# Optimization experiments

Measured on AMD Instinct MI355X. Metric: run time of the kernel, lower is better.

## Reference

```python
import jax, jax.numpy as jnp
import numpy as np
import math

B, T, E = 1, 2048, 1024
H = 8                      # num_heads
D = E // H // 2            # head_dim = 64
LAMBDA_INIT = 0.8 - 0.6 * math.exp(-0.3 * 1)  # depth=1
SCALE_BASE = 512.0
THETA = 10000.0


def _rope_tables(T, d):
    # lucidrains rotary-embedding-torch, use_xpos=True, interleaved pairs
    inv_freq = 1.0 / (THETA ** (jnp.arange(0, d, 2, dtype=jnp.float32) / d))
    pos = jnp.arange(T, dtype=jnp.float32)
    freqs = pos[:, None] * inv_freq[None, :]            # (T, d/2)
    freqs = jnp.repeat(freqs, 2, axis=-1)               # (T, d) interleaved
    sv = (jnp.arange(0, d, 2, dtype=jnp.float32) + 0.4 * d) / (1.4 * d)
    power = (pos - T // 2) / SCALE_BASE
    scale = sv[None, :] ** power[:, None]               # (T, d/2)
    scale = jnp.concatenate([scale, scale], axis=-1)    # (T, d)
    return freqs, scale


def _rotate_half(x):
    # interleaved rotate: (..., d) pairs (x1, x2) -> (-x2, x1)
    x1 = x[..., 0::2]
    x2 = x[..., 1::2]
    return jnp.stack([-x2, x1], axis=-1).reshape(x.shape)


def _apply_rope(t, freqs, scale):
    # t: (B, T, h, d); freqs/scale: (T, d) broadcast over heads
    f = freqs[None, :, None, :]
    s = scale[None, :, None, :]
    return t * jnp.cos(f) * s + _rotate_half(t) * jnp.sin(f) * s


def setup_inputs() -> dict:
    key = jax.random.key(0)
    ks = jax.random.split(key, 9)
    w = 0.02
    return {
        "x": jax.random.normal(ks[0], (B, T, E), dtype=jnp.float32),
        "Wq": jax.random.normal(ks[1], (E, E), dtype=jnp.float32) * w,
        "Wk": jax.random.normal(ks[2], (E, E), dtype=jnp.float32) * w,
        "Wv": jax.random.normal(ks[3], (E, E), dtype=jnp.float32) * w,
        "Wo": jax.random.normal(ks[4], (E, E), dtype=jnp.float32) * w,
        "lambda_q1": jax.random.normal(ks[5], (D,), dtype=jnp.float32) * 0.1,
        "lambda_k1": jax.random.normal(ks[6], (D,), dtype=jnp.float32) * 0.1,
        "lambda_q2": jax.random.normal(ks[7], (D,), dtype=jnp.float32) * 0.1,
        "lambda_k2": jax.random.normal(ks[8], (D,), dtype=jnp.float32) * 0.1,
    }


def reference(x, Wq, Wk, Wv, Wo, lambda_q1, lambda_k1, lambda_q2, lambda_k2):
    b, t, e = x.shape
    scaling = D ** -0.5

    q = (x @ Wq.T).reshape(b, t, 2 * H, D)
    k = (x @ Wk.T).reshape(b, t, 2 * H, D)   # n_rep = 1
    v = (x @ Wv.T).reshape(b, t, H, 2 * D)

    freqs, scale = _rope_tables(t, D)
    q = _apply_rope(q, freqs, scale)
    k = _apply_rope(k, freqs, 1.0 / scale)   # xpos: keys use scale**-1

    q = jnp.transpose(q, (0, 2, 1, 3)) * scaling   # (B, 2H, T, D)
    k = jnp.transpose(k, (0, 2, 1, 3))             # (B, 2H, T, D)
    v = jnp.transpose(v, (0, 2, 1, 3))             # (B, H, T, 2D)

    scores = jnp.einsum('bhtd,bhsd->bhts', q, k)
    probs = jax.nn.softmax(scores.astype(jnp.float32), axis=-1).astype(scores.dtype)

    lam1 = jnp.exp(jnp.sum(lambda_q1 * lambda_k1))
    lam2 = jnp.exp(jnp.sum(lambda_q2 * lambda_k2))
    lam = lam1 - lam2 + LAMBDA_INIT

    probs = probs.reshape(b, H, 2, t, t)
    diff = probs[:, :, 0] - lam * probs[:, :, 1]   # (B, H, T, T)

    attn = jnp.einsum('bhts,bhsd->bhtd', diff, v)  # (B, H, T, 2D)
    # RMSNorm (no affine), eps=1e-5
    attn = attn * jax.lax.rsqrt(jnp.mean(attn * attn, axis=-1, keepdims=True) + 1e-5)
    attn = attn * (1.0 - LAMBDA_INIT)

    attn = jnp.transpose(attn, (0, 2, 1, 3)).reshape(b, t, e)
    return attn @ Wo.T
```

## Files before the change

kernel.cpp:

```cpp
#include <hip/hip_runtime.h>
#include <hip/hip_bf16.h>

typedef __hip_bfloat16 bf16;
typedef _Float16 f16;
typedef __attribute__((ext_vector_type(8))) __bf16 bf16x8;
typedef __attribute__((ext_vector_type(8))) _Float16 f16x8;
typedef __attribute__((ext_vector_type(4))) _Float16 f16x4;
typedef __attribute__((ext_vector_type(4))) float floatx4;
typedef __attribute__((ext_vector_type(16))) float floatx16;

#define T_SEQ 2048
#define EMB   1024
#define LAMBDA_INIT 0.35550906759096926f

__device__ __forceinline__ bf16 f2bf(float f) {
  unsigned u;
  __builtin_memcpy(&u, &f, 4);
  u += 0x7FFF + ((u >> 16) & 1);
  unsigned short h = (unsigned short)(u >> 16);
  bf16 r;
  __builtin_memcpy(&r, &h, 2);
  return r;
}

__device__ __forceinline__ int cvtpk_bf16(float lo, float hi) {
  int r;
  asm("v_cvt_pk_bf16_f32 %0, %1, %2" : "=v"(r) : "v"(lo), "v"(hi));
  return r;
}

__device__ __forceinline__ void permswap(int& a, int& b) {
  asm volatile("v_permlane32_swap_b32 %0, %1" : "+v"(a), "+v"(b));
}

__device__ __forceinline__ void gl_lds16(const void* g, void* l) {
  __builtin_amdgcn_global_load_lds((const __attribute__((address_space(1))) void*)g,
                                   (__attribute__((address_space(3))) void*)l, 16, 0, 0);
}

__device__ __forceinline__ floatx4 mfma_h(f16x8 a, f16x8 b, floatx4 c) {
  return __builtin_amdgcn_mfma_f32_16x16x32_f16(a, b, c, 0, 0, 0);
}
__device__ __forceinline__ floatx16 mfma32_h(f16x8 a, f16x8 b, floatx16 c) {
  return __builtin_amdgcn_mfma_f32_32x32x16_f16(a, b, c, 0, 0, 0);
}
__device__ __forceinline__ floatx16 mfma32_bf(bf16x8 a, bf16x8 b, floatx16 c) {
  return __builtin_amdgcn_mfma_f32_32x32x16_bf16(a, b, c, 0, 0, 0);
}

__global__ __launch_bounds__(256) void convert_kernel(
    const float* __restrict__ x,  const float* __restrict__ wq,
    const float* __restrict__ wk, const float* __restrict__ wv,
    const float* __restrict__ wo,
    f16* __restrict__ xf, f16* __restrict__ wqf, f16* __restrict__ wkf,
    f16* __restrict__ wvf, f16* __restrict__ wof)
{
  int b = blockIdx.x;
  const float* src; f16* dst; long off;
  if      (b < 2048) { src = x;  dst = xf;  off = (long)b * 1024; }
  else if (b < 3072) { src = wq; dst = wqf; off = (long)(b - 2048) * 1024; }
  else if (b < 4096) { src = wk; dst = wkf; off = (long)(b - 3072) * 1024; }
  else if (b < 5120) { src = wv; dst = wvf; off = (long)(b - 4096) * 1024; }
  else               { src = wo; dst = wof; off = (long)(b - 5120) * 1024; }
  long i = off + threadIdx.x * 4;
  float4 v = *(const float4*)(src + i);
  f16x4 o;
  o.x = (f16)v.x; o.y = (f16)v.y; o.z = (f16)v.z; o.w = (f16)v.w;
  *(f16x4*)(dst + i) = o;
}

template <int MODE>
__device__ __forceinline__ void gemm64x128_f16(
    const f16* __restrict__ A_, const f16* __restrict__ B_,
    void* C0v, int K, int ldc, int m0, int n0, char* smem)
{
  f16* As = (f16*)smem;
  f16* Bs = (f16*)(smem + 8192);
  const int tid  = threadIdx.x;
  const int wave = tid >> 6, lane = tid & 63, quad = lane >> 4, l16 = lane & 15;
  const int mo = (wave & 1) << 5;
  const int no = (wave >> 1) << 6;

  floatx4 acc[2][4];
  #pragma unroll
  for (int i = 0; i < 2; i++)
    #pragma unroll
    for (int j = 0; j < 4; j++) { acc[i][j][0]=0.f; acc[i][j][1]=0.f; acc[i][j][2]=0.f; acc[i][j][3]=0.f; }

  const int srow = tid >> 3;
  const int ch   = (tid & 7) ^ (srow & 7);
  const long aoff = (long)(m0 + srow) * K + ch * 8;
  const long boff = (long)(n0 + srow) * K + ch * 8;
  const int wb = wave << 10;

  for (int k0 = 0; k0 < K; k0 += 64) {
    #pragma unroll
    for (int rr = 0; rr < 2; rr++)
      gl_lds16(A_ + aoff + k0 + (long)rr * 32 * K, smem + wb + rr * 4096);
    #pragma unroll
    for (int rr = 0; rr < 4; rr++)
      gl_lds16(B_ + boff + k0 + (long)rr * 32 * K, smem + 8192 + wb + rr * 4096);
    __syncthreads();
    #pragma unroll
    for (int kt = 0; kt < 2; kt++) {
      f16x8 a[2], b[4];
      #pragma unroll
      for (int i = 0; i < 2; i++) {
        int m = mo + i * 16 + l16;
        a[i] = *(const f16x8*)(As + m * 64 + ((((kt << 2) | quad) ^ (m & 7)) << 3));
      }
      #pragma unroll
      for (int j = 0; j < 4; j++) {
        int n = no + j * 16 + l16;
        b[j] = *(const f16x8*)(Bs + n * 64 + ((((kt << 2) | quad) ^ (n & 7)) << 3));
      }
      #pragma unroll
      for (int i = 0; i < 2; i++)
        #pragma unroll
        for (int j = 0; j < 4; j++)
          acc[i][j] = mfma_h(a[i], b[j], acc[i][j]);
    }
    __syncthreads();
  }

  if (MODE == 1) {
    #pragma unroll
    for (int i = 0; i < 2; i++)
      #pragma unroll
      for (int j = 0; j < 4; j++)
        #pragma unroll
        for (int r = 0; r < 4; r++) {
          int row = m0 + mo + i * 16 + quad * 4 + r;
          int col = n0 + no + j * 16 + l16;
          ((float*)C0v)[(long)row * ldc + col] = acc[i][j][r];
        }
  } else {
    unsigned short* E = (unsigned short*)smem;
    #pragma unroll
    for (int i = 0; i < 2; i++)
      #pragma unroll
      for (int j = 0; j < 4; j++)
        #pragma unroll
        for (int r = 0; r < 4; r++) {
          int row = mo + i * 16 + quad * 4 + r;
          int col = no + j * 16 + l16;
          float v = acc[i][j][r];
          unsigned short bits;
          if (MODE == 0) {
            bf16 t = f2bf(v);
            __builtin_memcpy(&bits, &t, 2);
          } else {
            float p = __shfl_xor(v, 1, 64);
            int d = col & 63;
            float fr = (float)(m0 + row) * __expf((float)(d >> 1) * -0.28782313662425574f);
            float sn, cs;
            sincosf(fr, &sn, &cs);
            float rot = (col & 1) ? fmaf(v, cs, p * sn) : fmaf(v, cs, -p * sn);
            float power = (float)(m0 + row - 1024) * (1.0f / 512.0f);
            if (MODE == 3) power = -power;
            float sv = fmaf(2.0f, (float)(d & 31), 25.6f) * (1.0f / 89.6f);
            float s = __expf(power * __logf(sv));
            float ov = rot * s;
            if (MODE == 2) ov *= 0.125f;
            f16 t = (f16)ov;
            __builtin_memcpy(&bits, &t, 2);
          }
          E[row * 128 + col] = bits;
        }
    __syncthreads();
    const int rr0 = tid >> 4;
    const int c8  = (tid & 15) * 8;
    #pragma unroll
    for (int p2 = 0; p2 < 4; p2++) {
      int row = p2 * 16 + rr0;
      *(uint4*)((unsigned short*)C0v + (long)(m0 + row) * ldc + n0 + c8) =
          *(const uint4*)(E + row * 128 + c8);
    }
  }
}

__global__ __launch_bounds__(256) void qkv_gemm(
    const f16* __restrict__ xf,
    const f16* __restrict__ wqf, const f16* __restrict__ wkf,
    const f16* __restrict__ wvf,
    f16* __restrict__ qf, f16* __restrict__ kf, bf16* __restrict__ vt)
{
  __shared__ char smem[24576];
  int bid = blockIdx.x;
  if (bid < 256) {
    gemm64x128_f16<2>(xf, wqf, qf, 1024, 1024, (bid >> 3) * 64, (bid & 7) * 128, smem);
  } else if (bid < 512) {
    bid -= 256;
    gemm64x128_f16<3>(xf, wkf, kf, 1024, 1024, (bid >> 3) * 64, (bid & 7) * 128, smem);
  } else {
    bid -= 512;
    gemm64x128_f16<0>(wvf, xf, vt, 1024, 2048, (bid >> 4) * 64, (bid & 15) * 128, smem);
  }
}

__global__ __launch_bounds__(256) void out_gemm(const f16* __restrict__ attn,
                                                const f16* __restrict__ Wo,
                                                float* __restrict__ out)
{
  __shared__ char smem[24576];
  gemm64x128_f16<1>(attn, Wo, out, 1024, 1024,
                    (blockIdx.x >> 3) * 64, (blockIdx.x & 7) * 128, smem);
}

__global__ __launch_bounds__(256) void diff_attn(
    const f16* __restrict__ qf_, const f16* __restrict__ kf_,
    const bf16* __restrict__ vt,
    const float* __restrict__ lq1, const float* __restrict__ lk1,
    const float* __restrict__ lq2, const float* __restrict__ lk2,
    f16* __restrict__ attn)
{
  __shared__ char smem[65536];
  const int tid  = threadIdx.x;
  const int wave = tid >> 6, lane = tid & 63;
  const int l32 = lane & 31, lh = lane >> 5;
  const int h  = blockIdx.x & 7;
  const int qb = blockIdx.x >> 3;
  const int hl = wave >> 1;
  const int ws = wave & 1;
  const int hh = h * 2 + hl;
  const int t0 = qb * 32;

  float a1 = lq1[lane] * lk1[lane];
  float a2 = lq2[lane] * lk2[lane];
  #pragma unroll
  for (int off = 1; off < 64; off <<= 1) {
    a1 += __shfl_xor(a1, off, 64);
    a2 += __shfl_xor(a2, off, 64);
  }
  const float lam = __expf(a1) - __expf(a2) + LAMBDA_INIT;

  f16x8 qfr[4];
  {
    const f16* qrow = qf_ + (long)(t0 + l32) * EMB + hh * 64 + lh * 8;
    #pragma unroll
    for (int kt = 0; kt < 4; kt++) qfr[kt] = *(const f16x8*)(qrow + kt * 16);
  }

  floatx16 o[4];
  #pragma unroll
  for (int nt = 0; nt < 4; nt++)
    #pragma unroll
    for (int r = 0; r < 16; r++) o[nt][r] = 0.f;
  float lr0 = 0.f, lr1 = 0.f, lr2 = 0.f, lr3 = 0.f;

  const int srow = lane >> 3;
  const int ch   = (lane & 7) ^ srow;
  const f16*  kgp = kf_ + (long)(h * 2 + ws) * 64 + (long)srow * EMB + ch * 8;
  const bf16* vgp = vt + (long)(h * 128 + (wave - 2) * 64 + srow) * T_SEQ + ch * 8;
  const int kofs = wave * 8192;
  const int vofs = 16384 + (wave - 2) * 8192;

  if (wave < 2) {
    #pragma unroll
    for (int j = 0; j < 8; j++)
      gl_lds16(kgp + (long)j * 8 * EMB, smem + kofs + j * 1024);
  } else {
    #pragma unroll
    for (int j = 0; j < 8; j++)
      gl_lds16(vgp + (long)j * 8 * T_SEQ, smem + vofs + j * 1024);
  }

  for (int kb = 0; kb < T_SEQ; kb += 64) {
    const int cur = (kb >> 6) & 1;
    const char* sb = smem + cur * 32768;

    asm volatile("s_waitcnt vmcnt(0)" ::: "memory");
    asm volatile("s_barrier" ::: "memory");

    const f16*  Ks  = (const f16*)(sb + hl * 8192);
    const bf16* Vsb = (const bf16*)(sb + 16384);

    f16x8 kfr[4];
    #pragma unroll
    for (int kt = 0; kt < 4; kt++) {
      int krow = ws * 32 + l32;
      int c = kt * 2 + lh;
      kfr[kt] = *(const f16x8*)(Ks + krow * 64 + ((c ^ (krow & 7)) << 3));
    }
    bf16x8 vfr[4][2];
    #pragma unroll
    for (int nt = 0; nt < 4; nt++) {
      #pragma unroll
      for (int kt = 0; kt < 2; kt++) {
        int vrow = nt * 32 + l32;
        int c = ws * 4 + kt * 2 + lh;
        vfr[nt][kt] = *(const bf16x8*)(Vsb + vrow * 64 + ((c ^ (vrow & 7)) << 3));
      }
    }

    if (kb + 64 < T_SEQ) {
      char* nb = smem + (cur ^ 1) * 32768;
      if (wave < 2) {
        #pragma unroll
        for (int j = 0; j < 8; j++)
          gl_lds16(kgp + (long)(kb + 64) * EMB + (long)j * 8 * EMB,
                   nb + kofs + j * 1024);
      } else {
        #pragma unroll
        for (int j = 0; j < 8; j++)
          gl_lds16(vgp + (kb + 64) + (long)j * 8 * T_SEQ,
                   nb + vofs + j * 1024);
      }
    }

    floatx16 s;
    #pragma unroll
    for (int r = 0; r < 16; r++) s[r] = 0.f;
    #pragma unroll
    for (int kt = 0; kt < 4; kt++)
      s = mfma32_h(kfr[kt], qfr[kt], s);
    #pragma unroll
    for (int r = 0; r < 4; r++) {
      float p0 = __builtin_amdgcn_exp2f(
          fmaf(s[r], 1.4426950408889634f, -17.312340490667562f));
      float p1 = __builtin_amdgcn_exp2f(
          fmaf(s[r + 4], 1.4426950408889634f, -17.312340490667562f));
      float p2 = __builtin_amdgcn_exp2f(
          fmaf(s[r + 8], 1.4426950408889634f, -17.312340490667562f));
      float p3 = __builtin_amdgcn_exp2f(
          fmaf(s[r + 12], 1.4426950408889634f, -17.312340490667562f));
      s[r] = p0; s[r + 4] = p1; s[r + 8] = p2; s[r + 12] = p3;
      lr0 += p0; lr1 += p1; lr2 += p2; lr3 += p3;
    }
    bf16x8 pf[2];
    #pragma unroll
    for (int kt = 0; kt < 2; kt++) {
      const int b0 = kt * 8;
      int w0 = cvtpk_bf16(s[b0 + 0], s[b0 + 1]);
      int w1 = cvtpk_bf16(s[b0 + 2], s[b0 + 3]);
      int w2 = cvtpk_bf16(s[b0 + 4], s[b0 + 5]);
      int w3 = cvtpk_bf16(s[b0 + 6], s[b0 + 7]);
      permswap(w0, w2);
      permswap(w1, w3);
      union { int i[4]; bf16x8 v; } u;
      u.i[0] = w0; u.i[1] = w1; u.i[2] = w2; u.i[3] = w3;
      pf[kt] = u.v;
    }
    #pragma unroll
    for (int nt = 0; nt < 4; nt++) {
      #pragma unroll
      for (int kt = 0; kt < 2; kt++)
        o[nt] = mfma32_bf(pf[kt], vfr[nt][kt], o[nt]);
    }
  }
  __syncthreads();

  float lr = (lr0 + lr1) + (lr2 + lr3);
  float lrw = lr + __shfl_xor(lr, 32, 64);

  float* Cb = (float*)smem;
  float* Lb = (float*)(smem + 32768);

  if (ws == 1) {
    #pragma unroll
    for (int r = 0; r < 16; r++) {
      int m = (r & 3) + 8 * (r >> 2) + 4 * lh;
      #pragma unroll
      for (int nt = 0; nt < 4; nt++)
        Cb[hl * 4096 + m * 128 + nt * 32 + l32] = o[nt][r];
    }
  }
  if (lh == 0) Lb[ws * 64 + hl * 32 + l32] = lrw;
  __syncthreads();
  if (ws == 0) {
    #pragma unroll
    for (int r = 0; r < 16; r++) {
      int m = (r & 3) + 8 * (r >> 2) + 4 * lh;
      float inv = 1.0f / (Lb[hl * 32 + m] + Lb[64 + hl * 32 + m]);
      #pragma unroll
      for (int nt = 0; nt < 4; nt++)
        o[nt][r] = (o[nt][r] + Cb[hl * 4096 + m * 128 + nt * 32 + l32]) * inv;
    }
  }
  __syncthreads();
  if (hl == 1 && ws == 0) {
    #pragma unroll
    for (int r = 0; r < 16; r++) {
      int m = (r & 3) + 8 * (r >> 2) + 4 * lh;
      #pragma unroll
      for (int nt = 0; nt < 4; nt++)
        Cb[4096 + m * 128 + nt * 32 + l32] = o[nt][r];
    }
  }
  __syncthreads();
  if (hl == 0 && ws == 0) {
    float ss[16];
    #pragma unroll
    for (int r = 0; r < 16; r++) {
      int m = (r & 3) + 8 * (r >> 2) + 4 * lh;
      ss[r] = 0.f;
      #pragma unroll
      for (int nt = 0; nt < 4; nt++) {
        float v = o[nt][r] - lam * Cb[4096 + m * 128 + nt * 32 + l32];
        o[nt][r] = v;
        ss[r] += v * v;
      }
    }
    #pragma unroll
    for (int r = 0; r < 16; r++) {
      ss[r] += __shfl_xor(ss[r], 1, 64);
      ss[r] += __shfl_xor(ss[r], 2, 64);
      ss[r] += __shfl_xor(ss[r], 4, 64);
      ss[r] += __shfl_xor(ss[r], 8, 64);
      ss[r] += __shfl_xor(ss[r], 16, 64);
      float rms = rsqrtf(ss[r] * (1.0f / 128.0f) + 1e-5f) * (1.0f - LAMBDA_INIT);
      int m = (r & 3) + 8 * (r >> 2) + 4 * lh;
      #pragma unroll
      for (int nt = 0; nt < 4; nt++)
        attn[(long)(t0 + m) * EMB + h * 128 + nt * 32 + l32] = (f16)(o[nt][r] * rms);
    }
  }
}

extern "C" void kernel_launch(void* const* d_in, const int* in_sizes, int n_in,
                              void* d_out, int out_size, void* d_ws, size_t ws_size,
                              hipStream_t stream)
{
  (void)in_sizes; (void)n_in; (void)out_size; (void)ws_size;
  const float* x   = (const float*)d_in[0];
  const float* Wq  = (const float*)d_in[1];
  const float* Wk  = (const float*)d_in[2];
  const float* Wv  = (const float*)d_in[3];
  const float* Wo  = (const float*)d_in[4];
  const float* lq1 = (const float*)d_in[5];
  const float* lk1 = (const float*)d_in[6];
  const float* lq2 = (const float*)d_in[7];
  const float* lk2 = (const float*)d_in[8];
  float* out = (float*)d_out;

  const size_t TM = (size_t)T_SEQ * EMB;
  const size_t WM = (size_t)EMB * EMB;
  bf16* vtws = (bf16*)d_ws;
  f16*  aws  = (f16*)(vtws + TM);
  f16*  xf   = aws  + TM;
  f16*  wqf  = xf   + TM;
  f16*  wkf  = wqf  + WM;
  f16*  wvf  = wkf  + WM;
  f16*  wof  = wvf  + WM;
  f16*  qf   = wof  + WM;
  f16*  kf   = qf   + TM;

  convert_kernel<<<6144, 256, 0, stream>>>(x, Wq, Wk, Wv, Wo,
                                           xf, wqf, wkf, wvf, wof);
  qkv_gemm<<<768, 256, 0, stream>>>(xf, wqf, wkf, wvf, qf, kf, vtws);
  diff_attn<<<512, 256, 0, stream>>>(qf, kf, vtws, lq1, lk1, lq2, lk2, aws);
  out_gemm<<<256, 256, 0, stream>>>(aws, wof, out);
}
```

Before: 172.7 us.

## Use 128x128 double-buffered direct-to-LDS tiles for QKV projection GEMM

Adds a new 128x128 GEMM tile routine for the QKV projection. It uses BK=64, a swizzled LDS layout, global-to-LDS async loads and double buffering across k-steps, with the RoPE/xpos epilogue kept. The goal is to raise data reuse per block and overlap loads with MFMA work, halving the grid to 384 blocks. In exchange it uses 64KB of LDS and more accumulators per block, which may lower occupancy and gives fewer blocks to spread over the CUs.

```diff
diff --git a/kernel.cpp b/kernel.cpp
--- a/kernel.cpp
+++ b/kernel.cpp
@@ -134,67 +134,140 @@
           int col = n0 + no + j * 16 + l16;
           ((float*)C0v)[(long)row * ldc + col] = acc[i][j][r];
         }
-  } else {
-    unsigned short* E = (unsigned short*)smem;
-    #pragma unroll
-    for (int i = 0; i < 2; i++)
-      #pragma unroll
-      for (int j = 0; j < 4; j++)
+  }
+}
+
+template <int MODE>
+__device__ __forceinline__ void gemm128x128_f16(
+    const f16* __restrict__ A_, const f16* __restrict__ B_,
+    void* C0v, int K, int ldc, int m0, int n0, char* smem)
+{
+  const int tid  = threadIdx.x;
+  const int wave = tid >> 6, lane = tid & 63, quad = lane >> 4, l16 = lane & 15;
+  const int mo = wave << 5;
+
+  floatx4 acc[2][8];
+  #pragma unroll
+  for (int i = 0; i < 2; i++)
+    #pragma unroll
+    for (int j = 0; j < 8; j++) { acc[i][j][0]=0.f; acc[i][j][1]=0.f; acc[i][j][2]=0.f; acc[i][j][3]=0.f; }
+
+  const int srow = tid >> 3;
+  const int ch   = (tid & 7) ^ (srow & 7);
+  const long aoff = (long)(m0 + srow) * K + ch * 8;
+  const long boff = (long)(n0 + srow) * K + ch * 8;
+  const int wb = wave << 10;
+
+  #pragma unroll
+  for (int j = 0; j < 4; j++) {
+    gl_lds16(A_ + aoff + (long)j * 32 * K, smem + j * 4096 + wb);
+    gl_lds16(B_ + boff + (long)j * 32 * K, smem + 16384 + j * 4096 + wb);
+  }
+
+  for (int k0 = 0; k0 < K; k0 += 64) {
+    const int cur = (k0 >> 6) & 1;
+    const char* sb = smem + cur * 32768;
+
+    asm volatile("s_waitcnt vmcnt(0)" ::: "memory");
+    asm volatile("s_barrier" ::: "memory");
+
+    const f16* As = (const f16*)sb;
+    const f16* Bs = (const f16*)(sb + 16384);
+
+    f16x8 a[2][2], b[2][8];
+    #pragma unroll
+    for (int kt = 0; kt < 2; kt++) {
+      #pragma unroll
+      for (int i = 0; i < 2; i++) {
+        int m = mo + i * 16 + l16;
+        a[kt][i] = *(const f16x8*)(As + m * 64 + ((((kt << 2) | quad) ^ (m & 7)) << 3));
+      }
+      #pragma unroll
+      for (int j = 0; j < 8; j++) {
+        int n = j * 16 + l16;
+        b[kt][j] = *(const f16x8*)(Bs + n * 64 + ((((kt << 2) | quad) ^ (n & 7)) << 3));
+      }
+    }
+
+    if (k0 + 64 < K) {
+      char* nb = smem + (cur ^ 1) * 32768;
+      #pragma unroll
+      for (int j = 0; j < 4; j++) {
+        gl_lds16(A_ + aoff + k0 + 64 + (long)j * 32 * K, nb + j * 4096 + wb);
+        gl_lds16(B_ + boff + k0 + 64 + (long)j * 32 * K, nb + 16384 + j * 4096 + wb);
+      }
+    }
+
+    #pragma unroll
+    for (int kt = 0; kt < 2; kt++)
+      #pragma unroll
+      for (int i = 0; i < 2; i++)
         #pragma unroll
-        for (int r = 0; r < 4; r++) {
-          int row = mo + i * 16 + quad * 4 + r;
-          int col = no + j * 16 + l16;
-          float v = acc[i][j][r];
-          unsigned short bits;
-          if (MODE == 0) {
-            bf16 t = f2bf(v);
-            __builtin_memcpy(&bits, &t, 2);
-          } else {
-            float p = __shfl_xor(v, 1, 64);
-            int d = col & 63;
-            float fr = (float)(m0 + row) * __expf((float)(d >> 1) * -0.28782313662425574f);
-            float sn, cs;
-            sincosf(fr, &sn, &cs);
-            float rot = (col & 1) ? fmaf(v, cs, p * sn) : fmaf(v, cs, -p * sn);
-            float power = (float)(m0 + row - 1024) * (1.0f / 512.0f);
-            if (MODE == 3) power = -power;
-            float sv = fmaf(2.0f, (float)(d & 31), 25.6f) * (1.0f / 89.6f);
-            float s = __expf(power * __logf(sv));
-            float ov = rot * s;
-            if (MODE == 2) ov *= 0.125f;
-            f16 t = (f16)ov;
-            __builtin_memcpy(&bits, &t, 2);
-          }
-          E[row * 128 + col] = bits;
+        for (int j = 0; j < 8; j++)
+          acc[i][j] = mfma_h(a[kt][i], b[kt][j], acc[i][j]);
+  }
+  __syncthreads();
+
+  unsigned short* E = (unsigned short*)smem;
+  #pragma unroll
+  for (int i = 0; i < 2; i++)
+    #pragma unroll
+    for (int j = 0; j < 8; j++)
+      #pragma unroll
+      for (int r = 0; r < 4; r++) {
+        int row = mo + i * 16 + quad * 4 + r;
+        int col = j * 16 + l16;
+        float v = acc[i][j][r];
+        unsigned short bits;
+        if (MODE == 0) {
+          bf16 t = f2bf(v);
+          __builtin_memcpy(&bits, &t, 2);
+        } else {
+          float p = __shfl_xor(v, 1, 64);
+          int gcol = n0 + col;
+          int d = gcol & 63;
+          float fr = (float)(m0 + row) * __expf((float)(d >> 1) * -0.28782313662425574f);
+          float sn, cs;
+          sincosf(fr, &sn, &cs);
+          float rot = (gcol & 1) ? fmaf(v, cs, p * sn) : fmaf(v, cs, -p * sn);
+          float power = (float)(m0 + row - 1024) * (1.0f / 512.0f);
+          if (MODE == 3) power = -power;
+          float sv = fmaf(2.0f, (float)(d & 31), 25.6f) * (1.0f / 89.6f);
+          float s = __expf(power * __logf(sv));
+          float ov = rot * s;
+          if (MODE == 2) ov *= 0.125f;
+          f16 t = (f16)ov;
+          __builtin_memcpy(&bits, &t, 2);
         }
-    __syncthreads();
-    const int rr0 = tid >> 4;
-    const int c8  = (tid & 15) * 8;
-    #pragma unroll
-    for (int p2 = 0; p2 < 4; p2++) {
-      int row = p2 * 16 + rr0;
-      *(uint4*)((unsigned short*)C0v + (long)(m0 + row) * ldc + n0 + c8) =
-          *(const uint4*)(E + row * 128 + c8);
-    }
-  }
-}
-
-__global__ __launch_bounds__(256) void qkv_gemm(
+        E[row * 128 + col] = bits;
+      }
+  __syncthreads();
+  const int rr0 = tid >> 4;
+  const int c8  = (tid & 15) * 8;
+  #pragma unroll
+  for (int p2 = 0; p2 < 8; p2++) {
+    int row = p2 * 16 + rr0;
+    *(uint4*)((unsigned short*)C0v + (long)(m0 + row) * ldc + n0 + c8) =
+        *(const uint4*)(E + row * 128 + c8);
+  }
+}
+
+__global__ __launch_bounds__(256, 2) void qkv_gemm(
     const f16* __restrict__ xf,
     const f16* __restrict__ wqf, const f16* __restrict__ wkf,
     const f16* __restrict__ wvf,
     f16* __restrict__ qf, f16* __restrict__ kf, bf16* __restrict__ vt)
 {
-  __shared__ char smem[24576];
+  __shared__ char smem[65536];
   int bid = blockIdx.x;
-  if (bid < 256) {
-    gemm64x128_f16<2>(xf, wqf, qf, 1024, 1024, (bid >> 3) * 64, (bid & 7) * 128, smem);
-  } else if (bid < 512) {
+  if (bid < 128) {
+    gemm128x128_f16<2>(xf, wqf, qf, 1024, 1024, (bid >> 3) * 128, (bid & 7) * 128, smem);
+  } else if (bid < 256) {
+    bid -= 128;
+    gemm128x128_f16<3>(xf, wkf, kf, 1024, 1024, (bid >> 3) * 128, (bid & 7) * 128, smem);
+  } else {
     bid -= 256;
-    gemm64x128_f16<3>(xf, wkf, kf, 1024, 1024, (bid >> 3) * 64, (bid & 7) * 128, smem);
-  } else {
-    bid -= 512;
-    gemm64x128_f16<0>(wvf, xf, vt, 1024, 2048, (bid >> 4) * 64, (bid & 15) * 128, smem);
+    gemm128x128_f16<0>(wvf, xf, vt, 1024, 2048, (bid >> 4) * 128, (bid & 15) * 128, smem);
   }
 }
 
@@ -447,7 +520,7 @@
 
   convert_kernel<<<6144, 256, 0, stream>>>(x, Wq, Wk, Wv, Wo,
                                            xf, wqf, wkf, wvf, wof);
-  qkv_gemm<<<768, 256, 0, stream>>>(xf, wqf, wkf, wvf, qf, kf, vtws);
+  qkv_gemm<<<384, 256, 0, stream>>>(xf, wqf, wkf, wvf, qf, kf, vtws);
   diff_attn<<<512, 256, 0, stream>>>(qf, kf, vtws, lq1, lk1, lq2, lk2, aws);
   out_gemm<<<256, 256, 0, stream>>>(aws, wof, out);
 }
```

After: 181.1 us. 1.05x slower.

## Split output projection GEMM along K into two partials plus add kernel

Applied to the files above, without the earlier changes.

The output projection GEMM is split along the reduction dimension into two halves. This doubles the block count from 256 to 512, each block doing half the K loop and writing an fp32 partial into reused workspace (the x/Wq/Wk and q/k buffers). A separate elementwise kernel then sums the two partials into the output. The aim is more parallelism and shorter per-block latency on a small GEMM, at the cost of an extra launch and extra fp32 traffic to write and re-read the partials.

```diff
diff --git a/kernel.cpp b/kernel.cpp
--- a/kernel.cpp
+++ b/kernel.cpp
@@ -72,7 +72,7 @@
 template <int MODE>
 __device__ __forceinline__ void gemm64x128_f16(
     const f16* __restrict__ A_, const f16* __restrict__ B_,
-    void* C0v, int K, int ldc, int m0, int n0, char* smem)
+    void* C0v, int Kld, int Klen, int ldc, int m0, int n0, char* smem)
 {
   f16* As = (f16*)smem;
   f16* Bs = (f16*)(smem + 8192);
@@ -89,17 +89,17 @@
 
   const int srow = tid >> 3;
   const int ch   = (tid & 7) ^ (srow & 7);
-  const long aoff = (long)(m0 + srow) * K + ch * 8;
-  const long boff = (long)(n0 + srow) * K + ch * 8;
+  const long aoff = (long)(m0 + srow) * Kld + ch * 8;
+  const long boff = (long)(n0 + srow) * Kld + ch * 8;
   const int wb = wave << 10;
 
-  for (int k0 = 0; k0 < K; k0 += 64) {
+  for (int k0 = 0; k0 < Klen; k0 += 64) {
     #pragma unroll
     for (int rr = 0; rr < 2; rr++)
-      gl_lds16(A_ + aoff + k0 + (long)rr * 32 * K, smem + wb + rr * 4096);
+      gl_lds16(A_ + aoff + k0 + (long)rr * 32 * Kld, smem + wb + rr * 4096);
     #pragma unroll
     for (int rr = 0; rr < 4; rr++)
-      gl_lds16(B_ + boff + k0 + (long)rr * 32 * K, smem + 8192 + wb + rr * 4096);
+      gl_lds16(B_ + boff + k0 + (long)rr * 32 * Kld, smem + 8192 + wb + rr * 4096);
     __syncthreads();
     #pragma unroll
     for (int kt = 0; kt < 2; kt++) {
@@ -188,23 +188,40 @@
   __shared__ char smem[24576];
   int bid = blockIdx.x;
   if (bid < 256) {
-    gemm64x128_f16<2>(xf, wqf, qf, 1024, 1024, (bid >> 3) * 64, (bid & 7) * 128, smem);
+    gemm64x128_f16<2>(xf, wqf, qf, 1024, 1024, 1024, (bid >> 3) * 64, (bid & 7) * 128, smem);
   } else if (bid < 512) {
     bid -= 256;
-    gemm64x128_f16<3>(xf, wkf, kf, 1024, 1024, (bid >> 3) * 64, (bid & 7) * 128, smem);
+    gemm64x128_f16<3>(xf, wkf, kf, 1024, 1024, 1024, (bid >> 3) * 64, (bid & 7) * 128, smem);
   } else {
     bid -= 512;
-    gemm64x128_f16<0>(wvf, xf, vt, 1024, 2048, (bid >> 4) * 64, (bid & 15) * 128, smem);
+    gemm64x128_f16<0>(wvf, xf, vt, 1024, 1024, 2048, (bid >> 4) * 64, (bid & 15) * 128, smem);
   }
 }
 
 __global__ __launch_bounds__(256) void out_gemm(const f16* __restrict__ attn,
                                                 const f16* __restrict__ Wo,
-                                                float* __restrict__ out)
+                                                float* __restrict__ p0,
+                                                float* __restrict__ p1)
 {
   __shared__ char smem[24576];
-  gemm64x128_f16<1>(attn, Wo, out, 1024, 1024,
-                    (blockIdx.x >> 3) * 64, (blockIdx.x & 7) * 128, smem);
+  int bid = blockIdx.x;
+  const int kh = bid >> 8;
+  const int b  = bid & 255;
+  float* pb = kh ? p1 : p0;
+  gemm64x128_f16<1>(attn + kh * 512, Wo + kh * 512, pb, 1024, 512, 1024,
+                    (b >> 3) * 64, (b & 7) * 128, smem);
+}
+
+__global__ __launch_bounds__(256) void add_out(const float* __restrict__ p0,
+                                               const float* __restrict__ p1,
+                                               float* __restrict__ out)
+{
+  long i = ((long)blockIdx.x * 256 + threadIdx.x) * 4;
+  float4 a = *(const float4*)(p0 + i);
+  float4 b = *(const float4*)(p1 + i);
+  float4 c;
+  c.x = a.x + b.x; c.y = a.y + b.y; c.z = a.z + b.z; c.w = a.w + b.w;
+  *(float4*)(out + i) = c;
 }
 
 __global__ __launch_bounds__(256) void diff_attn(
@@ -445,9 +462,13 @@
   f16*  qf   = wof  + WM;
   f16*  kf   = qf   + TM;
 
+  float* p0 = (float*)xf;
+  float* p1 = (float*)qf;
+
   convert_kernel<<<6144, 256, 0, stream>>>(x, Wq, Wk, Wv, Wo,
                                            xf, wqf, wkf, wvf, wof);
   qkv_gemm<<<768, 256, 0, stream>>>(xf, wqf, wkf, wvf, qf, kf, vtws);
   diff_attn<<<512, 256, 0, stream>>>(qf, kf, vtws, lq1, lk1, lq2, lk2, aws);
-  out_gemm<<<256, 256, 0, stream>>>(aws, wof, out);
-}
+  out_gemm<<<512, 256, 0, stream>>>(aws, wof, p0, p1);
+  add_out<<<2048, 256, 0, stream>>>(p0, p1, out);
+}
```

Measured after the change: 170.7 us, median of 2. No clear change (-1.1%).
